# Kernel tuning notes

Hardware: AMD Instinct MI355X
Metric: run time of the kernel (lower is better)

Reference implementation:

```python
import jax, jax.numpy as jnp
import numpy as np
import math

N_HEADS = 16


def _rope(t, cos, sin):
    # t: [B, S, H, d_k] with d_k paired as (even, odd) -> complex multiply by cos+i*sin
    B, S, H, dk = t.shape
    t = t.reshape(B, S, H, dk // 2, 2)
    t0, t1 = t[..., 0], t[..., 1]
    c = cos[None, :S, None, :]
    s = sin[None, :S, None, :]
    out = jnp.stack([t0 * c - t1 * s, t0 * s + t1 * c], axis=-1)
    return out.reshape(B, S, H, dk)


def setup_inputs() -> dict:
    key = jax.random.key(0)
    ks = jax.random.split(key, 6)
    B, S, D = 2, 2048, 2048
    dk = D // N_HEADS  # 128
    x = jax.random.normal(ks[0], (B, S, D), dtype=jnp.float32)
    # standard RoPE angle table
    inv_freq = 1.0 / (10000.0 ** (np.arange(0, dk, 2, dtype=np.float32) / dk))  # [dk/2]
    t = np.arange(S, dtype=np.float32)
    ang = np.outer(t, inv_freq)  # [S, dk/2]
    freqs_cos = jnp.asarray(np.cos(ang), dtype=jnp.float32)
    freqs_sin = jnp.asarray(np.sin(ang), dtype=jnp.float32)
    # additive causal mask [1,1,S,S]
    causal = jnp.tril(jnp.ones((S, S), dtype=bool))
    mask = jnp.where(causal, 0.0, -1e9).astype(jnp.float32)[None, None]
    wscale = 1.0 / math.sqrt(D)
    Wq = jax.random.normal(ks[1], (D, D), dtype=jnp.float32) * wscale
    Wk = jax.random.normal(ks[2], (D, D), dtype=jnp.float32) * wscale
    Wv = jax.random.normal(ks[3], (D, D), dtype=jnp.float32) * wscale
    Wo = jax.random.normal(ks[4], (D, D), dtype=jnp.float32) * wscale
    return {"x": x, "freqs_cos": freqs_cos, "freqs_sin": freqs_sin, "mask": mask,
            "Wq": Wq, "Wk": Wk, "Wv": Wv, "Wo": Wo}


def reference(x, freqs_cos, freqs_sin, mask, Wq, Wk, Wv, Wo):
    B, S, D = x.shape
    H = N_HEADS
    dk = D // H
    scale = math.sqrt(dk)
    # nn.Linear(w) applies x @ w.T
    Q = (x @ Wq.T).reshape(B, S, H, dk)
    K = (x @ Wk.T).reshape(B, S, H, dk)
    V = (x @ Wv.T).reshape(B, S, H, dk)
    Q = _rope(Q, freqs_cos, freqs_sin)
    K = _rope(K, freqs_cos, freqs_sin)
    new_kv_cache = (K, V)  # kv_cache=None path: cache is just current K, V
    # [B, H, S, dk]
    Qh = Q.transpose(0, 2, 1, 3)
    Kh = K.transpose(0, 2, 1, 3)
    Vh = V.transpose(0, 2, 1, 3)
    scores = jnp.einsum('bhqd,bhkd->bhqk', Qh, Kh) / scale + mask
    attn = jax.nn.softmax(scores, axis=-1)  # dropout=0 (eval)
    ctx = jnp.einsum('bhqk,bhkd->bhqd', attn, Vh)
    ctx = ctx.transpose(0, 2, 1, 3).reshape(B, S, D)
    output = ctx @ Wo.T
    return output, new_kv_cache[0], new_kv_cache[1]
```

## Files before the change

kernel.cpp:

```cpp
#include <hip/hip_runtime.h>
#include <hip/hip_bf16.h>

#define SEQ   2048
#define DIM   2048
#define NH    16
#define DKH   128
#define BATCH 2
#define MROWS (BATCH * SEQ)
#define NQT   (SEQ / 64)

using bf16 = __hip_bfloat16;
typedef __attribute__((ext_vector_type(8))) short short8;
typedef __attribute__((ext_vector_type(4))) short short4v;
typedef __attribute__((ext_vector_type(4))) float floatx4;

union BfBits { bf16 h; short s; };

__device__ __forceinline__ void gl_lds16(const bf16* g, bf16* l) {
  __builtin_amdgcn_global_load_lds(
      (__attribute__((address_space(1))) void*)(g),
      (__attribute__((address_space(3))) void*)(l), 16, 0, 0);
}

#define S_BAR  __builtin_amdgcn_s_barrier()
#define VMCNT6 do { asm volatile("s_waitcnt vmcnt(6)" ::: "memory"); __builtin_amdgcn_sched_barrier(0); } while (0)
#define VMCNT0 do { asm volatile("s_waitcnt vmcnt(0)" ::: "memory"); __builtin_amdgcn_sched_barrier(0); } while (0)
#define LGKM0  do { asm volatile("s_waitcnt lgkmcnt(0)" ::: "memory"); __builtin_amdgcn_sched_barrier(0); } while (0)

__global__ __launch_bounds__(256) void cast5_kernel(const float* __restrict__ x,
                                                    const float* __restrict__ wq,
                                                    const float* __restrict__ wk,
                                                    const float* __restrict__ wv,
                                                    const float* __restrict__ wo,
                                                    bf16* __restrict__ dst,
                                                    int nX4, int nW4, int nTot) {
  int i = blockIdx.x * 256 + threadIdx.x;
  if (i >= nTot) return;
  const float* src;
  int off;
  int j = i - nX4;
  if (j < 0) { src = x; off = i; }
  else {
    int wsel = j >> 20;
    off = j & (nW4 - 1);
    src = (wsel == 0) ? wq : (wsel == 1) ? wk : (wsel == 2) ? wv : wo;
  }
  float4 v = reinterpret_cast<const float4*>(src)[off];
  __hip_bfloat162 h01, h23;
  h01.x = __float2bfloat16(v.x); h01.y = __float2bfloat16(v.y);
  h23.x = __float2bfloat16(v.z); h23.y = __float2bfloat16(v.w);
  reinterpret_cast<__hip_bfloat162*>(dst)[i * 2 + 0] = h01;
  reinterpret_cast<__hip_bfloat162*>(dst)[i * 2 + 1] = h23;
}

template <int ROWS>
__device__ __forceinline__ void stage_swz(const bf16* __restrict__ G, bf16* lds,
                                          int row0, int k0, int w, int l) {
  const int rr = w * 8 + (l >> 3);
  const int cc = ((l & 7) * 8) ^ ((l >> 3) * 8);
#pragma unroll
  for (int u = 0; u < ROWS / 64; ++u)
    gl_lds16(G + (size_t)(row0 + u * 64 + rr) * DIM + k0 + cc,
             lds + (u * 64 + w * 8) * 64);
}

template <int MODE>
__global__ __launch_bounds__(512, 2) void gemm256(const bf16* __restrict__ A,
                                                  const bf16* __restrict__ Bw,
                                                  bf16* __restrict__ Qraw,
                                                  float* __restrict__ Kout,
                                                  float* __restrict__ Vout) {
  __shared__ bf16 smem[2 * 256 * 64 + 2 * 128 * 64];
  bf16* LA = smem;
  bf16* LB = smem + 2 * 256 * 64;

  const int t = threadIdx.x;
  const int w = t >> 6, l = t & 63;
  const int lr = l & 15, quad = l >> 4;
  const int wr = w >> 2;
  const int wc = w & 3;
  const int m0 = blockIdx.y * 256;
  const int n0g = blockIdx.x * 128;

  const int cb = ((quad * 8) ^ ((lr & 7) * 8));

  floatx4 acc[8][2];
#pragma unroll
  for (int mi = 0; mi < 8; ++mi)
#pragma unroll
    for (int nj = 0; nj < 2; ++nj) acc[mi][nj] = (floatx4){0.f, 0.f, 0.f, 0.f};

  const int NT = DIM / 64;

  stage_swz<256>(A, LA, m0, 0, w, l);
  stage_swz<128>(Bw, LB, n0g, 0, w, l);
  stage_swz<256>(A, LA + 256 * 64, m0, 64, w, l);
  stage_swz<128>(Bw, LB + 128 * 64, n0g, 64, w, l);
  VMCNT6;
  S_BAR;

  int cur = 0;
  for (int kt = 0; kt < NT; ++kt) {
    const bf16* la = LA + cur * (256 * 64);
    const bf16* lb = LB + cur * (128 * 64);

    short8 bfr[2][2];
#pragma unroll
    for (int nj = 0; nj < 2; ++nj) {
      int rb = (wc * 32 + nj * 16 + lr) * 64;
      bfr[nj][0] = *reinterpret_cast<const short8*>(lb + rb + cb);
      bfr[nj][1] = *reinterpret_cast<const short8*>(lb + rb + (cb ^ 32));
    }

#pragma unroll
    for (int qp = 0; qp < 4; ++qp) {
      short8 af[4][2];
#pragma unroll
      for (int i = 0; i < 4; ++i) {
        int ra = (wr * 128 + (qp * 4 + i) * 16 + lr) * 64;
        af[i][0] = *reinterpret_cast<const short8*>(la + ra + cb);
        af[i][1] = *reinterpret_cast<const short8*>(la + ra + (cb ^ 32));
      }
      LGKM0;
      __builtin_amdgcn_s_setprio(1);
#pragma unroll
      for (int i = 0; i < 4; ++i)
#pragma unroll
        for (int nj = 0; nj < 2; ++nj) {
          acc[qp * 4 + i][nj] = __builtin_amdgcn_mfma_f32_16x16x32_bf16(
              af[i][0], bfr[nj][0], acc[qp * 4 + i][nj], 0, 0, 0);
          acc[qp * 4 + i][nj] = __builtin_amdgcn_mfma_f32_16x16x32_bf16(
              af[i][1], bfr[nj][1], acc[qp * 4 + i][nj], 0, 0, 0);
        }
      __builtin_amdgcn_s_setprio(0);
    }

    S_BAR;
    if (kt + 2 < NT) {
      stage_swz<256>(A, LA + cur * (256 * 64), m0, (kt + 2) * 64, w, l);
      stage_swz<128>(Bw, LB + cur * (128 * 64), n0g, (kt + 2) * 64, w, l);
      VMCNT6;
    } else {
      VMCNT0;
    }
    S_BAR;
    cur ^= 1;
  }

#pragma unroll
  for (int mi = 0; mi < 8; ++mi)
#pragma unroll
    for (int nj = 0; nj < 2; ++nj) {
      int rg = m0 + wr * 128 + mi * 16 + quad * 4;
      if constexpr (MODE == 0) {
        const int region = n0g >> 11;
        int lcol = (n0g & 2047) + wc * 32 + nj * 16 + lr;
#pragma unroll
        for (int rr2 = 0; rr2 < 4; ++rr2) {
          size_t idx = (size_t)(rg + rr2) * DIM + lcol;
          if (region == 0)      Qraw[idx] = __float2bfloat16(acc[mi][nj][rr2]);
          else if (region == 1) Kout[idx] = acc[mi][nj][rr2];
          else                  Vout[idx] = acc[mi][nj][rr2];
        }
      } else {
        int lcol = n0g + wc * 32 + nj * 16 + lr;
#pragma unroll
        for (int rr2 = 0; rr2 < 4; ++rr2)
          Kout[(size_t)(rg + rr2) * DIM + lcol] = acc[mi][nj][rr2];
      }
    }
}

__global__ __launch_bounds__(256) void rope_q(const bf16* __restrict__ Qraw,
                                              const float* __restrict__ cosT,
                                              const float* __restrict__ sinT,
                                              bf16* __restrict__ Qb) {
  int g = blockIdx.x * 256 + threadIdx.x;
  int p = g & 63;
  int r = g >> 6;
  int h = r & 15;
  int s = (r >> 4) & (SEQ - 1);
  int b = r >> 15;
  __hip_bfloat162 v = reinterpret_cast<const __hip_bfloat162*>(Qraw)[g];
  float x0 = __bfloat162float(v.x), x1 = __bfloat162float(v.y);
  float c = cosT[s * 64 + p], sn = sinT[s * 64 + p];
  __hip_bfloat162 o;
  o.x = __float2bfloat16(x0 * c - x1 * sn);
  o.y = __float2bfloat16(x0 * sn + x1 * c);
  reinterpret_cast<__hip_bfloat162*>(Qb)[((size_t)(b * NH + h) * SEQ + s) * 64 + p] = o;
}

__global__ __launch_bounds__(256) void rope_k(float* __restrict__ Kf,
                                              const float* __restrict__ cosT,
                                              const float* __restrict__ sinT,
                                              bf16* __restrict__ Kb) {
  int g = blockIdx.x * 256 + threadIdx.x;
  int p = g & 63;
  int r = g >> 6;
  int h = r & 15;
  int s = (r >> 4) & (SEQ - 1);
  int b = r >> 15;
  float2 v = reinterpret_cast<const float2*>(Kf)[g];
  float c = cosT[s * 64 + p], sn = sinT[s * 64 + p];
  float o0 = v.x * c - v.y * sn;
  float o1 = v.x * sn + v.y * c;
  reinterpret_cast<float2*>(Kf)[g] = make_float2(o0, o1);
  __hip_bfloat162 ob;
  ob.x = __float2bfloat16(o0);
  ob.y = __float2bfloat16(o1);
  reinterpret_cast<__hip_bfloat162*>(Kb)[((size_t)(b * NH + h) * SEQ + s) * 64 + p] = ob;
}

__global__ __launch_bounds__(256) void vt_kernel(const float* __restrict__ V,
                                                 bf16* __restrict__ Vt) {
  __shared__ float tile[32][33];
  const int s0 = blockIdx.x * 32;
  const int d0 = blockIdx.y * 32;
  const int bh = blockIdx.z;
  const int b = bh >> 4, h = bh & 15;
  const int t = threadIdx.x;
  const int row = t >> 3, c4 = (t & 7) * 4;

  float4 v = *reinterpret_cast<const float4*>(
      V + (size_t)(b * SEQ + s0 + row) * DIM + h * DKH + d0 + c4);
  tile[row][c4 + 0] = v.x; tile[row][c4 + 1] = v.y;
  tile[row][c4 + 2] = v.z; tile[row][c4 + 3] = v.w;
  __syncthreads();

  short4v ov;
#pragma unroll
  for (int i = 0; i < 4; ++i) {
    BfBits u; u.h = __float2bfloat16(tile[c4 + i][row]);
    ov[i] = u.s;
  }
  *reinterpret_cast<short4v*>(Vt + ((size_t)(b * NH + h) * DKH + d0 + row) * SEQ + s0 + c4) = ov;
}

__global__ __launch_bounds__(256) void attn_mfma(const bf16* __restrict__ Qb,
                                                 const bf16* __restrict__ Kb,
                                                 const bf16* __restrict__ Vt,
                                                 bf16* __restrict__ ctx) {
  const int bx = blockIdx.x;
  const int h = blockIdx.y;
  const int b = blockIdx.z;
  const int t = threadIdx.x;
  const int w = t >> 6, lane = t & 63;
  const int lr = lane & 15, quad = lane >> 4;

  __shared__ short Ks[64 * 136];
  __shared__ short Vs[128 * 72];
  __shared__ short Ps[4 * 16 * 72];

  const float scale2 = 0.08838834764831845f * 1.44269504f;
  const float THR = 11.5413f;
  const size_t headQK = (size_t)(b * NH + h) * SEQ * DKH;

  for (int pass = 0; pass < 2; ++pass) {
    const int qt = pass ? bx : (NQT - 1 - bx);

    short8 qa[4];
    {
      const short* qbase = (const short*)Qb + headQK + (size_t)(qt * 64 + w * 16 + lr) * DKH;
#pragma unroll
      for (int kk = 0; kk < 4; ++kk)
        qa[kk] = *reinterpret_cast<const short8*>(qbase + kk * 32 + quad * 8);
    }

    floatx4 o[8];
#pragma unroll
    for (int n = 0; n < 8; ++n) o[n] = (floatx4){0.f, 0.f, 0.f, 0.f};
    float m[4] = {-1e30f, -1e30f, -1e30f, -1e30f};
    float l[4] = {0.f, 0.f, 0.f, 0.f};

    for (int kt = 0; kt <= qt; ++kt) {
      {
        const short* kbase = (const short*)Kb + headQK + (size_t)(kt * 64) * DKH;
#pragma unroll
        for (int u = 0; u < 4; ++u) {
          int c = t + 256 * u;
          *reinterpret_cast<int4*>(Ks + (c >> 4) * 136 + (c & 15) * 8) =
              *reinterpret_cast<const int4*>(kbase + c * 8);
        }
        const short* vbase = (const short*)Vt + (size_t)(b * NH + h) * DKH * SEQ + kt * 64;
#pragma unroll
        for (int u = 0; u < 4; ++u) {
          int c = t + 256 * u;
          *reinterpret_cast<int4*>(Vs + (c >> 3) * 72 + (c & 7) * 8) =
              *reinterpret_cast<const int4*>(vbase + (size_t)(c >> 3) * SEQ + (c & 7) * 8);
        }
      }
      __syncthreads();

      floatx4 sj[4];
#pragma unroll
      for (int j = 0; j < 4; ++j) sj[j] = (floatx4){0.f, 0.f, 0.f, 0.f};
#pragma unroll
      for (int j = 0; j < 4; ++j)
#pragma unroll
        for (int kk = 0; kk < 4; ++kk) {
          short8 kb = *reinterpret_cast<const short8*>(Ks + (j * 16 + lr) * 136 + kk * 32 + quad * 8);
          sj[j] = __builtin_amdgcn_mfma_f32_16x16x32_bf16(qa[kk], kb, sj[j], 0, 0, 0);
        }

      float sc[4][4];
#pragma unroll
      for (int j = 0; j < 4; ++j)
#pragma unroll
        for (int r = 0; r < 4; ++r) sc[j][r] = sj[j][r] * scale2;
      if (kt == qt) {
#pragma unroll
        for (int j = 0; j < 4; ++j) {
          int col = kt * 64 + j * 16 + lr;
#pragma unroll
          for (int r = 0; r < 4; ++r) {
            int rowg = qt * 64 + w * 16 + quad * 4 + r;
            if (col > rowg) sc[j][r] = -1e9f;
          }
        }
      }

#pragma unroll
      for (int r = 0; r < 4; ++r) {
        float mx = fmaxf(fmaxf(sc[0][r], sc[1][r]), fmaxf(sc[2][r], sc[3][r]));
        mx = fmaxf(mx, __shfl_xor(mx, 1, 16));
        mx = fmaxf(mx, __shfl_xor(mx, 2, 16));
        mx = fmaxf(mx, __shfl_xor(mx, 4, 16));
        mx = fmaxf(mx, __shfl_xor(mx, 8, 16));
        if (!__all(mx - m[r] <= THR)) {
          float mnew = fmaxf(m[r], mx);
          float alpha = __builtin_amdgcn_exp2f(m[r] - mnew);
          l[r] *= alpha;
#pragma unroll
          for (int n = 0; n < 8; ++n) o[n][r] *= alpha;
          m[r] = mnew;
        }
        float rs = 0.f;
#pragma unroll
        for (int j = 0; j < 4; ++j) {
          float p = __builtin_amdgcn_exp2f(sc[j][r] - m[r]);
          rs += p;
          BfBits u; u.h = __float2bfloat16(p);
          Ps[(w * 16 + quad * 4 + r) * 72 + j * 16 + lr] = u.s;
        }
        rs += __shfl_xor(rs, 1, 16);
        rs += __shfl_xor(rs, 2, 16);
        rs += __shfl_xor(rs, 4, 16);
        rs += __shfl_xor(rs, 8, 16);
        l[r] += rs;
      }

      short8 pa0 = *reinterpret_cast<const short8*>(Ps + (w * 16 + lr) * 72 + quad * 8);
      short8 pa1 = *reinterpret_cast<const short8*>(Ps + (w * 16 + lr) * 72 + 32 + quad * 8);
#pragma unroll
      for (int n = 0; n < 8; ++n) {
        short8 vb0 = *reinterpret_cast<const short8*>(Vs + (n * 16 + lr) * 72 + quad * 8);
        short8 vb1 = *reinterpret_cast<const short8*>(Vs + (n * 16 + lr) * 72 + 32 + quad * 8);
        o[n] = __builtin_amdgcn_mfma_f32_16x16x32_bf16(pa0, vb0, o[n], 0, 0, 0);
        o[n] = __builtin_amdgcn_mfma_f32_16x16x32_bf16(pa1, vb1, o[n], 0, 0, 0);
      }
      __syncthreads();
    }

    float inv[4];
#pragma unroll
    for (int r = 0; r < 4; ++r) inv[r] = 1.0f / l[r];
#pragma unroll
    for (int r = 0; r < 4; ++r) {
      size_t mrow = (size_t)b * SEQ + qt * 64 + w * 16 + quad * 4 + r;
      bf16* dst = ctx + mrow * DIM + h * DKH;
#pragma unroll
      for (int n = 0; n < 8; ++n)
        dst[n * 16 + lr] = __float2bfloat16(o[n][r] * inv[r]);
    }
  }
}

extern "C" void kernel_launch(void* const* d_in, const int* in_sizes, int n_in,
                              void* d_out, int out_size, void* d_ws, size_t ws_size,
                              hipStream_t stream) {
  const float* x = (const float*)d_in[0];
  const float* fcos = (const float*)d_in[1];
  const float* fsin = (const float*)d_in[2];
  const float* Wq = (const float*)d_in[4];
  const float* Wk = (const float*)d_in[5];
  const float* Wv = (const float*)d_in[6];
  const float* Wo = (const float*)d_in[7];

  float* out = (float*)d_out;
  float* Kout = out + (size_t)MROWS * DIM;
  float* Vout = Kout + (size_t)MROWS * DIM;

  const size_t MD = (size_t)MROWS * DIM;
  const size_t DD = (size_t)DIM * DIM;
  bf16* xb   = (bf16*)d_ws;
  bf16* Wqb  = xb + MD;
  bf16* Wkb  = Wqb + DD;
  bf16* Wvb  = Wkb + DD;
  bf16* Wob  = Wvb + DD;
  bf16* Qraw = Wob + DD;
  bf16* Qb   = Qraw + MD;
  bf16* Kb   = Qb + MD;
  bf16* Vt   = Kb + MD;
  bf16* ctxb = Qraw;

  const int nXD4 = MROWS * DIM / 4;
  const int nWD4 = DIM * DIM / 4;
  const int nTot = nXD4 + 4 * nWD4;
  cast5_kernel<<<nTot / 256, 256, 0, stream>>>(x, Wq, Wk, Wv, Wo, xb, nXD4, nWD4, nTot);

  dim3 gq(3 * DIM / 128, MROWS / 256);
  gemm256<0><<<gq, 512, 0, stream>>>(xb, Wqb, Qraw, Kout, Vout);

  const int npairs = MROWS * DIM / 2;
  rope_q<<<npairs / 256, 256, 0, stream>>>(Qraw, fcos, fsin, Qb);
  rope_k<<<npairs / 256, 256, 0, stream>>>(Kout, fcos, fsin, Kb);

  dim3 gv(SEQ / 32, DKH / 32, BATCH * NH);
  vt_kernel<<<gv, 256, 0, stream>>>(Vout, Vt);

  dim3 ga(NQT / 2, NH, BATCH);
  attn_mfma<<<ga, 256, 0, stream>>>(Qb, Kb, Vt, ctxb);

  dim3 go(DIM / 128, MROWS / 256);
  gemm256<1><<<go, 512, 0, stream>>>(ctxb, Wob, (bf16*)nullptr, out, (float*)nullptr);
}
```

Measured before the change: 476.6 us.

## Triple-buffer GEMM LDS and interleave global prefetch with MFMA compute

The 256x128 projection GEMM moves from double- to triple-buffered LDS staging. The next-next K tile's global-to-LDS loads are now split into the A half and the B half, and each half is issued between fragment loads and MFMA batches instead of after a barrier. This drops one of the two barriers per K iteration and lets memory traffic overlap with compute. In exchange, LDS use per block rises by about half, which could limit occupancy, and the schedule relies on vmcnt-based waits staying correct.

Measured after the change: 468.7 us. Within noise of the previous version (-1.7%).

```diff
diff --git a/kernel.cpp b/kernel.cpp
--- a/kernel.cpp
+++ b/kernel.cpp
@@ -53,6 +53,8 @@
   reinterpret_cast<__hip_bfloat162*>(dst)[i * 2 + 1] = h23;
 }
 
+#define BUFE (256 * 64 + 128 * 64)
+
 template <int ROWS>
 __device__ __forceinline__ void stage_swz(const bf16* __restrict__ G, bf16* lds,
                                           int row0, int k0, int w, int l) {
@@ -70,9 +72,7 @@
                                                   bf16* __restrict__ Qraw,
                                                   float* __restrict__ Kout,
                                                   float* __restrict__ Vout) {
-  __shared__ bf16 smem[2 * 256 * 64 + 2 * 128 * 64];
-  bf16* LA = smem;
-  bf16* LB = smem + 2 * 256 * 64;
+  __shared__ bf16 smem[3 * BUFE];
 
   const int t = threadIdx.x;
   const int w = t >> 6, l = t & 63;
@@ -92,17 +92,18 @@
 
   const int NT = DIM / 64;
 
-  stage_swz<256>(A, LA, m0, 0, w, l);
-  stage_swz<128>(Bw, LB, n0g, 0, w, l);
-  stage_swz<256>(A, LA + 256 * 64, m0, 64, w, l);
-  stage_swz<128>(Bw, LB + 128 * 64, n0g, 64, w, l);
+  stage_swz<256>(A, smem, m0, 0, w, l);
+  stage_swz<128>(Bw, smem + 256 * 64, n0g, 0, w, l);
+  stage_swz<256>(A, smem + BUFE, m0, 64, w, l);
+  stage_swz<128>(Bw, smem + BUFE + 256 * 64, n0g, 64, w, l);
   VMCNT6;
   S_BAR;
 
-  int cur = 0;
   for (int kt = 0; kt < NT; ++kt) {
-    const bf16* la = LA + cur * (256 * 64);
-    const bf16* lb = LB + cur * (128 * 64);
+    const bf16* la = smem + (kt % 3) * BUFE;
+    const bf16* lb = la + 256 * 64;
+    bf16* stg = smem + ((kt + 2) % 3) * BUFE;
+    const bool do_stage = (kt + 2 < NT);
 
     short8 bfr[2][2];
 #pragma unroll
@@ -111,40 +112,49 @@
       bfr[nj][0] = *reinterpret_cast<const short8*>(lb + rb + cb);
       bfr[nj][1] = *reinterpret_cast<const short8*>(lb + rb + (cb ^ 32));
     }
-
-#pragma unroll
-    for (int qp = 0; qp < 4; ++qp) {
-      short8 af[4][2];
-#pragma unroll
-      for (int i = 0; i < 4; ++i) {
-        int ra = (wr * 128 + (qp * 4 + i) * 16 + lr) * 64;
-        af[i][0] = *reinterpret_cast<const short8*>(la + ra + cb);
-        af[i][1] = *reinterpret_cast<const short8*>(la + ra + (cb ^ 32));
-      }
-      LGKM0;
-      __builtin_amdgcn_s_setprio(1);
-#pragma unroll
-      for (int i = 0; i < 4; ++i)
-#pragma unroll
-        for (int nj = 0; nj < 2; ++nj) {
-          acc[qp * 4 + i][nj] = __builtin_amdgcn_mfma_f32_16x16x32_bf16(
-              af[i][0], bfr[nj][0], acc[qp * 4 + i][nj], 0, 0, 0);
-          acc[qp * 4 + i][nj] = __builtin_amdgcn_mfma_f32_16x16x32_bf16(
-              af[i][1], bfr[nj][1], acc[qp * 4 + i][nj], 0, 0, 0);
-        }
-      __builtin_amdgcn_s_setprio(0);
-    }
-
+    short8 af[4][2];
+#pragma unroll
+    for (int i = 0; i < 4; ++i) {
+      int ra = (wr * 128 + i * 16 + lr) * 64;
+      af[i][0] = *reinterpret_cast<const short8*>(la + ra + cb);
+      af[i][1] = *reinterpret_cast<const short8*>(la + ra + (cb ^ 32));
+    }
+    if (do_stage) stage_swz<256>(A, stg, m0, (kt + 2) * 64, w, l);
+    LGKM0;
+    __builtin_amdgcn_s_setprio(1);
+#pragma unroll
+    for (int i = 0; i < 4; ++i)
+#pragma unroll
+      for (int nj = 0; nj < 2; ++nj) {
+        acc[i][nj] = __builtin_amdgcn_mfma_f32_16x16x32_bf16(
+            af[i][0], bfr[nj][0], acc[i][nj], 0, 0, 0);
+        acc[i][nj] = __builtin_amdgcn_mfma_f32_16x16x32_bf16(
+            af[i][1], bfr[nj][1], acc[i][nj], 0, 0, 0);
+      }
+    __builtin_amdgcn_s_setprio(0);
+
+#pragma unroll
+    for (int i = 0; i < 4; ++i) {
+      int ra = (wr * 128 + (i + 4) * 16 + lr) * 64;
+      af[i][0] = *reinterpret_cast<const short8*>(la + ra + cb);
+      af[i][1] = *reinterpret_cast<const short8*>(la + ra + (cb ^ 32));
+    }
+    if (do_stage) stage_swz<128>(Bw, stg + 256 * 64, n0g, (kt + 2) * 64, w, l);
+    LGKM0;
+    __builtin_amdgcn_s_setprio(1);
+#pragma unroll
+    for (int i = 0; i < 4; ++i)
+#pragma unroll
+      for (int nj = 0; nj < 2; ++nj) {
+        acc[i + 4][nj] = __builtin_amdgcn_mfma_f32_16x16x32_bf16(
+            af[i][0], bfr[nj][0], acc[i + 4][nj], 0, 0, 0);
+        acc[i + 4][nj] = __builtin_amdgcn_mfma_f32_16x16x32_bf16(
+            af[i][1], bfr[nj][1], acc[i + 4][nj], 0, 0, 0);
+      }
+    __builtin_amdgcn_s_setprio(0);
+
+    if (do_stage) { VMCNT6; } else { VMCNT0; }
     S_BAR;
-    if (kt + 2 < NT) {
-      stage_swz<256>(A, LA + cur * (256 * 64), m0, (kt + 2) * 64, w, l);
-      stage_swz<128>(Bw, LB + cur * (128 * 64), n0g, (kt + 2) * 64, w, l);
-      VMCNT6;
-    } else {
-      VMCNT0;
-    }
-    S_BAR;
-    cur ^= 1;
   }
 
 #pragma unroll
```
